# Kernel optimization log

Measured on AMD Instinct MI355X. Metric: run time of the kernel, lower is better.

Reference implementation:

```python
import jax, jax.numpy as jnp
import numpy as np

B, T, C, K, NC = 256, 240, 512, 64, 4  # batch, chunk_size, dim, clusters, num_classes+1
EPS = 1e-12


def setup_inputs() -> dict:
    key = jax.random.key(0)
    k1, k2, k3, k4 = jax.random.split(key, 4)
    inputs = jax.random.normal(k1, (B, T, C), dtype=jnp.float32)
    conv_w = jax.random.normal(k2, (K, C), dtype=jnp.float32) * 0.05   # 1x1 assignment conv, no bias (vladv2=False)
    centroids = jax.random.normal(k3, (K, C), dtype=jnp.float32)
    fc_w = jax.random.normal(k4, (NC, K * C), dtype=jnp.float32) * 0.02
    fc_b = jnp.zeros((NC,), dtype=jnp.float32)
    return {"inputs": inputs, "conv_w": conv_w, "centroids": centroids, "fc_w": fc_w, "fc_b": fc_b}


def _l2norm(x, axis):
    return x / jnp.clip(jnp.linalg.norm(x, axis=axis, keepdims=True), EPS)


def reference(inputs, conv_w, centroids, fc_w, fc_b):
    # inputs: [B, T, C]. Torch permutes to NCHW=(B, C, T, 1); feature dim = C.
    x = _l2norm(inputs, axis=-1)                      # normalize_input over feature dim
    # soft assignment: 1x1 conv -> logits [B, T, K], softmax over clusters
    a = jax.nn.softmax(jnp.einsum('btc,kc->btk', x, conv_w), axis=-1)
    # vlad[b,k,c] = sum_t a[b,t,k] * (x[b,t,c] - centroids[k,c])
    #            = einsum(a, x) - (sum_t a) * centroids   (avoids [B,K,C,T] intermediate)
    vlad = jnp.einsum('btk,btc->bkc', a, x) - a.sum(axis=1)[:, :, None] * centroids[None]
    vlad = _l2norm(vlad, axis=-1)                     # intra-normalization over C
    v = vlad.reshape(vlad.shape[0], -1)               # [B, K*C]
    v = _l2norm(v, axis=-1)                           # final L2 normalize
    # dropout is identity in eval mode; fc + sigmoid
    return jax.nn.sigmoid(v @ fc_w.T + fc_b)
```

## Files before the change

### kernel.cpp

```cpp
#include <hip/hip_runtime.h>
#include <hip/hip_bf16.h>
#include <stdint.h>

#define BB 256
#define TT 240
#define CC 512
#define KK 64
#define NCLS 4
#define CHUNK 32
#define NCHUNK 8
#define THREADS 1024

typedef __attribute__((ext_vector_type(8))) short bf16x8;
typedef __attribute__((ext_vector_type(4))) float f32x4;

__device__ __forceinline__ unsigned short f2bf(float f) {
    union { float f; unsigned int i; } x; x.f = f;
    unsigned int r = x.i + 0x7FFFu + ((x.i >> 16) & 1u);
    return (unsigned short)(r >> 16);
}
__device__ __forceinline__ unsigned int pk2cvt(float lo, float hi) {
    union { __hip_bfloat162 h; unsigned int u; } c;
    c.h = __float22bfloat162_rn(float2{lo, hi});
    return c.u;
}
__device__ __forceinline__ void LB() {
    asm volatile("s_waitcnt lgkmcnt(0)\n\ts_barrier" ::: "memory");
}

struct alignas(16) SMemChunk {
    unsigned short x[CHUNK][520];
    unsigned short xT[CC][40];
    float logitsP[2][CHUNK][68];
    unsigned short aT[KK][40];
};
struct alignas(16) SMemEpi { unsigned short vbuf[KK * CC]; };
union SMemU { SMemChunk c; SMemEpi e; };

__global__ __launch_bounds__(THREADS, 4) void netvlad_kernel(
    const float* __restrict__ inp,
    const float* __restrict__ convw,
    const float* __restrict__ cent,
    const float* __restrict__ fcw,
    const float* __restrict__ fcb,
    float* __restrict__ out)
{
    __shared__ SMemU sm;
    __shared__ float sumsq_sh[CHUNK];
    __shared__ float asum[KK];
    __shared__ float ssred[4][KK];
    __shared__ float gred[16];
    __shared__ float fcred[16][NCLS];
    __shared__ float vinv_sh;

    const int tid  = threadIdx.x;
    const int b    = blockIdx.x;
    const int w    = tid >> 6;
    const int lane = tid & 63;
    const int grp  = (lane >> 4) & 3;
    const int col  = lane & 15;
    const int cg   = w & 3;
    const int th   = (w >> 2) & 1;
    const int kh   = w >> 3;
    const int cq   = w >> 2;

    if (tid < KK) asum[tid] = 0.f;

    f32x4 acc[8];
    #pragma unroll
    for (int j = 0; j < 8; ++j) acc[j] = (f32x4){0.f, 0.f, 0.f, 0.f};

    bf16x8 cw[8];
    #pragma unroll
    for (int s = 0; s < 8; ++s) {
        const float* p = convw + (size_t)(cg * 16 + col) * CC + (kh * 8 + s) * 32 + grp * 8;
        float4 a0 = *(const float4*)p;
        float4 a1 = *(const float4*)(p + 4);
        bf16x8 v;
        v[0] = (short)f2bf(a0.x); v[1] = (short)f2bf(a0.y);
        v[2] = (short)f2bf(a0.z); v[3] = (short)f2bf(a0.w);
        v[4] = (short)f2bf(a1.x); v[5] = (short)f2bf(a1.y);
        v[6] = (short)f2bf(a1.z); v[7] = (short)f2bf(a1.w);
        cw[s] = v;
    }

    const size_t ibase = (size_t)b * (TT * CC);

    float4 r0[2], r1[2];
    #pragma unroll
    for (int i = 0; i < 2; ++i) {
        int g = tid + i * THREADS;
        int t = g >> 6, c8 = (g & 63) << 3;
        const float* p = inp + ibase + (size_t)t * CC + c8;
        r0[i] = *(const float4*)p;
        r1[i] = *(const float4*)(p + 4);
    }

    for (int ch = 0; ch < NCHUNK; ++ch) {
        const int t0 = ch * CHUNK;
        const int tvalid = (TT - t0 < CHUNK) ? (TT - t0) : CHUNK;

        #pragma unroll
        for (int i = 0; i < 2; ++i) {
            int g = tid + i * THREADS;
            int t = g >> 6, c8 = (g & 63) << 3;
            float4 u0 = r0[i], u1 = r1[i];
            uint4 val = (uint4){pk2cvt(u0.x, u0.y), pk2cvt(u0.z, u0.w),
                                pk2cvt(u1.x, u1.y), pk2cvt(u1.z, u1.w)};
            float s = u0.x*u0.x + u0.y*u0.y + u0.z*u0.z + u0.w*u0.w
                    + u1.x*u1.x + u1.y*u1.y + u1.z*u1.z + u1.w*u1.w;
            if (t >= tvalid) { val = (uint4){0u,0u,0u,0u}; s = 0.f; }
            *(uint4*)&sm.c.x[t][c8] = val;
            s += __shfl_xor(s, 1);  s += __shfl_xor(s, 2);  s += __shfl_xor(s, 4);
            s += __shfl_xor(s, 8);  s += __shfl_xor(s, 16); s += __shfl_xor(s, 32);
            if (lane == 0) sumsq_sh[t] = s;
        }
        if (ch + 1 < NCHUNK) {
            int nt0 = t0 + CHUNK;
            #pragma unroll
            for (int i = 0; i < 2; ++i) {
                int g = tid + i * THREADS;
                int t = g >> 6, c8 = (g & 63) << 3;
                int gt = nt0 + t; if (gt > TT - 1) gt = TT - 1;
                const float* p = inp + ibase + (size_t)gt * CC + c8;
                r0[i] = *(const float4*)p;
                r1[i] = *(const float4*)(p + 4);
            }
        }
        LB();

        {
            int c = tid & 511, th2 = tid >> 9;
            #pragma unroll
            for (int tb2 = 0; tb2 < 2; ++tb2) {
                int tb = th2 * 2 + tb2;
                bf16x8 v;
                #pragma unroll
                for (int j = 0; j < 8; ++j) v[j] = (short)sm.c.x[tb * 8 + j][c];
                *(bf16x8*)&sm.c.xT[c][tb * 8] = v;
            }
        }
        {
            f32x4 lt = (f32x4){0.f, 0.f, 0.f, 0.f};
            #pragma unroll
            for (int s = 0; s < 8; ++s) {
                bf16x8 bb = *(const bf16x8*)&sm.c.x[th * 16 + col][(kh * 8 + s) * 32 + grp * 8];
                lt = __builtin_amdgcn_mfma_f32_16x16x32_bf16(cw[s], bb, lt, 0, 0, 0);
            }
            #pragma unroll
            for (int r = 0; r < 4; ++r)
                sm.c.logitsP[kh][th * 16 + col][cg * 16 + grp * 4 + r] = lt[r];
        }
        LB();

        if (tid < 512) {
            int t = tid >> 4, part = tid & 15;
            float rinv = 1.f / fmaxf(sqrtf(sumsq_sh[t]), 1e-12f);
            rinv = (t < tvalid) ? rinv : 0.f;

            float l[4]; float lmax = -1e30f;
            #pragma unroll
            for (int q = 0; q < 4; ++q) {
                l[q] = (sm.c.logitsP[0][t][q * 16 + part] +
                        sm.c.logitsP[1][t][q * 16 + part]) * rinv;
                lmax = fmaxf(lmax, l[q]);
            }
            lmax = fmaxf(lmax, __shfl_xor(lmax, 1));
            lmax = fmaxf(lmax, __shfl_xor(lmax, 2));
            lmax = fmaxf(lmax, __shfl_xor(lmax, 4));
            lmax = fmaxf(lmax, __shfl_xor(lmax, 8));
            float es = 0.f;
            #pragma unroll
            for (int q = 0; q < 4; ++q) { l[q] = __expf(l[q] - lmax); es += l[q]; }
            es += __shfl_xor(es, 1); es += __shfl_xor(es, 2);
            es += __shfl_xor(es, 4); es += __shfl_xor(es, 8);
            float is = 1.f / es;
            #pragma unroll
            for (int q = 0; q < 4; ++q) {
                float a = l[q] * is;
                sm.c.logitsP[0][t][q * 16 + part] = a;
                sm.c.aT[q * 16 + part][t] = (unsigned short)f2bf(a * rinv);
            }
        }
        LB();

        if (tid < KK) {
            float s = 0.f;
            for (int t = 0; t < tvalid; ++t) s += sm.c.logitsP[0][t][tid];
            asum[tid] += s;
        }
        {
            bf16x8 af = *(const bf16x8*)&sm.c.aT[cg * 16 + col][grp * 8];
            #pragma unroll
            for (int j = 0; j < 8; ++j) {
                bf16x8 bf = *(const bf16x8*)&sm.c.xT[cq * 128 + j * 16 + col][grp * 8];
                acc[j] = __builtin_amdgcn_mfma_f32_16x16x32_bf16(af, bf, acc[j], 0, 0, 0);
            }
        }
    }

    LB();

    #pragma unroll
    for (int r = 0; r < 4; ++r) {
        int cl = cg * 16 + grp * 4 + r;
        float as = asum[cl];
        float ss = 0.f;
        #pragma unroll
        for (int j = 0; j < 8; ++j) {
            int c = cq * 128 + j * 16 + col;
            float v = acc[j][r] - as * cent[(size_t)cl * CC + c];
            acc[j][r] = v;
            ss += v * v;
        }
        ss += __shfl_xor(ss, 1); ss += __shfl_xor(ss, 2);
        ss += __shfl_xor(ss, 4); ss += __shfl_xor(ss, 8);
        if (col == 0) ssred[cq][cl] = ss;
    }
    LB();

    float contrib = 0.f;
    #pragma unroll
    for (int r = 0; r < 4; ++r) {
        int cl = cg * 16 + grp * 4 + r;
        float ss = ssred[0][cl] + ssred[1][cl] + ssred[2][cl] + ssred[3][cl];
        float inv = 1.f / fmaxf(sqrtf(ss), 1e-12f);
        #pragma unroll
        for (int j = 0; j < 8; ++j) {
            float v = acc[j][r] * inv;
            acc[j][r] = v;
            contrib += v * v;
        }
    }
    #pragma unroll
    for (int m = 1; m < 64; m <<= 1) contrib += __shfl_xor(contrib, m);
    if (lane == 0) gred[w] = contrib;
    LB();
    if (tid == 0) {
        float tot = 0.f;
        #pragma unroll
        for (int i = 0; i < 16; ++i) tot += gred[i];
        vinv_sh = 1.f / fmaxf(sqrtf(tot), 1e-12f);
    }
    LB();

    {
        float vinv = vinv_sh;
        #pragma unroll
        for (int r = 0; r < 4; ++r) {
            int cl = cg * 16 + grp * 4 + r;
            #pragma unroll
            for (int j = 0; j < 8; ++j) {
                int c = cq * 128 + j * 16 + col;
                sm.e.vbuf[cl * CC + c] = f2bf(acc[j][r] * vinv);
            }
        }
    }
    LB();

    float pacc[NCLS] = {0.f, 0.f, 0.f, 0.f};
    #pragma unroll
    for (int i = 0; i < 4; ++i) {
        int idx = i * 8192 + tid * 8;
        bf16x8 vv = *(const bf16x8*)&sm.e.vbuf[idx];
        float vf[8];
        #pragma unroll
        for (int h = 0; h < 8; ++h) {
            union { unsigned int u; float f; } cvt;
            cvt.u = ((unsigned int)(unsigned short)vv[h]) << 16;
            vf[h] = cvt.f;
        }
        #pragma unroll
        for (int nc = 0; nc < NCLS; ++nc) {
            const float* wp = fcw + (size_t)nc * (KK * CC) + idx;
            float4 w0 = *(const float4*)wp;
            float4 w1 = *(const float4*)(wp + 4);
            pacc[nc] += vf[0] * w0.x + vf[1] * w0.y + vf[2] * w0.z + vf[3] * w0.w
                      + vf[4] * w1.x + vf[5] * w1.y + vf[6] * w1.z + vf[7] * w1.w;
        }
    }
    #pragma unroll
    for (int nc = 0; nc < NCLS; ++nc) {
        #pragma unroll
        for (int m = 1; m < 64; m <<= 1) pacc[nc] += __shfl_xor(pacc[nc], m);
    }
    if (lane == 0) {
        #pragma unroll
        for (int nc = 0; nc < NCLS; ++nc) fcred[w][nc] = pacc[nc];
    }
    LB();
    if (tid < NCLS) {
        float s = fcb[tid];
        #pragma unroll
        for (int ww = 0; ww < 16; ++ww) s += fcred[ww][tid];
        out[b * NCLS + tid] = 1.f / (1.f + __expf(-s));
    }
}

extern "C" void kernel_launch(void* const* d_in, const int* in_sizes, int n_in,
                              void* d_out, int out_size, void* d_ws, size_t ws_size,
                              hipStream_t stream) {
    const float* inp   = (const float*)d_in[0];
    const float* convw = (const float*)d_in[1];
    const float* cent  = (const float*)d_in[2];
    const float* fcw   = (const float*)d_in[3];
    const float* fcb   = (const float*)d_in[4];
    float* o = (float*)d_out;
    netvlad_kernel<<<BB, THREADS, 0, stream>>>(inp, convw, cent, fcw, fcb, o);
}
```

Baseline: 206.3 us.

## Use blocked LDS layout with transpose reads and double-buffered x tile

Replaces the explicit LDS transpose of the x chunk (x -> xT) with a blocked bf16 layout read through ds_read_b64_tr_b16 transpose loads for the aT·x MFMA. Double-buffers the x tile so the next chunk's store does not overwrite data still being read. Moves the per-row sum-of-squares reduction out of the load phase into the softmax threads, merged with the max shuffle reduction. This drops one LDS pass and a set of shuffles per chunk, at the cost of more complex addressing and inline asm that depends on the transpose-read instruction's semantics.

```diff
diff --git a/kernel.cpp b/kernel.cpp
--- a/kernel.cpp
+++ b/kernel.cpp
@@ -11,8 +11,13 @@
 #define NCHUNK 8
 #define THREADS 1024
 
+#define CBS 72
+#define TBS 2312
+#define XELEMS (8 * TBS)
+
 typedef __attribute__((ext_vector_type(8))) short bf16x8;
 typedef __attribute__((ext_vector_type(4))) float f32x4;
+typedef __attribute__((ext_vector_type(2))) unsigned int u32x2;
 
 __device__ __forceinline__ unsigned short f2bf(float f) {
     union { float f; unsigned int i; } x; x.f = f;
@@ -29,10 +34,10 @@
 }
 
 struct alignas(16) SMemChunk {
-    unsigned short x[CHUNK][520];
-    unsigned short xT[CC][40];
-    float logitsP[2][CHUNK][68];
+    unsigned short x[2][XELEMS];
+    float logitsP[2][CHUNK][67];
     unsigned short aT[KK][40];
+    float sumsqP[CHUNK][68];
 };
 struct alignas(16) SMemEpi { unsigned short vbuf[KK * CC]; };
 union SMemU { SMemChunk c; SMemEpi e; };
@@ -46,7 +51,6 @@
     float* __restrict__ out)
 {
     __shared__ SMemU sm;
-    __shared__ float sumsq_sh[CHUNK];
     __shared__ float asum[KK];
     __shared__ float ssred[4][KK];
     __shared__ float gred[16];
@@ -99,6 +103,8 @@
     for (int ch = 0; ch < NCHUNK; ++ch) {
         const int t0 = ch * CHUNK;
         const int tvalid = (TT - t0 < CHUNK) ? (TT - t0) : CHUNK;
+        const int buf = ch & 1;
+        unsigned short* xb = sm.c.x[buf];
 
         #pragma unroll
         for (int i = 0; i < 2; ++i) {
@@ -110,10 +116,9 @@
             float s = u0.x*u0.x + u0.y*u0.y + u0.z*u0.z + u0.w*u0.w
                     + u1.x*u1.x + u1.y*u1.y + u1.z*u1.z + u1.w*u1.w;
             if (t >= tvalid) { val = (uint4){0u,0u,0u,0u}; s = 0.f; }
-            *(uint4*)&sm.c.x[t][c8] = val;
-            s += __shfl_xor(s, 1);  s += __shfl_xor(s, 2);  s += __shfl_xor(s, 4);
-            s += __shfl_xor(s, 8);  s += __shfl_xor(s, 16); s += __shfl_xor(s, 32);
-            if (lane == 0) sumsq_sh[t] = s;
+            int off = (t >> 2) * TBS + (c8 >> 4) * CBS + (t & 3) * 16 + (c8 & 15);
+            *(uint4*)&xb[off] = val;
+            sm.c.sumsqP[t][lane] = s;
         }
         if (ch + 1 < NCHUNK) {
             int nt0 = t0 + CHUNK;
@@ -130,50 +135,45 @@
         LB();
 
         {
-            int c = tid & 511, th2 = tid >> 9;
-            #pragma unroll
-            for (int tb2 = 0; tb2 < 2; ++tb2) {
-                int tb = th2 * 2 + tb2;
-                bf16x8 v;
-                #pragma unroll
-                for (int j = 0; j < 8; ++j) v[j] = (short)sm.c.x[tb * 8 + j][c];
-                *(bf16x8*)&sm.c.xT[c][tb * 8] = v;
-            }
-        }
-        {
             f32x4 lt = (f32x4){0.f, 0.f, 0.f, 0.f};
+            const int t = th * 16 + col;
+            const int rb = (t >> 2) * TBS + (t & 3) * 16 + ((grp & 1) << 3);
             #pragma unroll
             for (int s = 0; s < 8; ++s) {
-                bf16x8 bb = *(const bf16x8*)&sm.c.x[th * 16 + col][(kh * 8 + s) * 32 + grp * 8];
+                const bf16x8 bb = *(const bf16x8*)&xb[rb + ((kh * 8 + s) * 2 + (grp >> 1)) * CBS];
                 lt = __builtin_amdgcn_mfma_f32_16x16x32_bf16(cw[s], bb, lt, 0, 0, 0);
             }
             #pragma unroll
             for (int r = 0; r < 4; ++r)
-                sm.c.logitsP[kh][th * 16 + col][cg * 16 + grp * 4 + r] = lt[r];
+                sm.c.logitsP[kh][t][cg * 16 + grp * 4 + r] = lt[r];
         }
         LB();
 
         if (tid < 512) {
             int t = tid >> 4, part = tid & 15;
-            float rinv = 1.f / fmaxf(sqrtf(sumsq_sh[t]), 1e-12f);
+            float4 sp = *(const float4*)&sm.c.sumsqP[t][part * 4];
+            float ss = sp.x + sp.y + sp.z + sp.w;
+
+            float l[4]; float lmax = -1e30f;
+            #pragma unroll
+            for (int q = 0; q < 4; ++q) {
+                l[q] = sm.c.logitsP[0][t][q * 16 + part] +
+                       sm.c.logitsP[1][t][q * 16 + part];
+                lmax = fmaxf(lmax, l[q]);
+            }
+            #pragma unroll
+            for (int m = 1; m < 16; m <<= 1) {
+                lmax = fmaxf(lmax, __shfl_xor(lmax, m));
+                ss  += __shfl_xor(ss, m);
+            }
+            float rinv = 1.f / fmaxf(sqrtf(ss), 1e-12f);
             rinv = (t < tvalid) ? rinv : 0.f;
-
-            float l[4]; float lmax = -1e30f;
-            #pragma unroll
-            for (int q = 0; q < 4; ++q) {
-                l[q] = (sm.c.logitsP[0][t][q * 16 + part] +
-                        sm.c.logitsP[1][t][q * 16 + part]) * rinv;
-                lmax = fmaxf(lmax, l[q]);
-            }
-            lmax = fmaxf(lmax, __shfl_xor(lmax, 1));
-            lmax = fmaxf(lmax, __shfl_xor(lmax, 2));
-            lmax = fmaxf(lmax, __shfl_xor(lmax, 4));
-            lmax = fmaxf(lmax, __shfl_xor(lmax, 8));
+            float m0 = lmax * rinv;
             float es = 0.f;
             #pragma unroll
-            for (int q = 0; q < 4; ++q) { l[q] = __expf(l[q] - lmax); es += l[q]; }
-            es += __shfl_xor(es, 1); es += __shfl_xor(es, 2);
-            es += __shfl_xor(es, 4); es += __shfl_xor(es, 8);
+            for (int q = 0; q < 4; ++q) { l[q] = __expf(l[q] * rinv - m0); es += l[q]; }
+            #pragma unroll
+            for (int m = 1; m < 16; m <<= 1) es += __shfl_xor(es, m);
             float is = 1.f / es;
             #pragma unroll
             for (int q = 0; q < 4; ++q) {
@@ -191,10 +191,27 @@
         }
         {
             bf16x8 af = *(const bf16x8*)&sm.c.aT[cg * 16 + col][grp * 8];
-            #pragma unroll
-            for (int j = 0; j < 8; ++j) {
-                bf16x8 bf = *(const bf16x8*)&sm.c.xT[cq * 128 + j * 16 + col][grp * 8];
-                acc[j] = __builtin_amdgcn_mfma_f32_16x16x32_bf16(af, bf, acc[j], 0, 0, 0);
+            unsigned xvb = (unsigned)(uintptr_t)&xb[(grp * 2) * TBS + (cq * 8) * CBS + col];
+            #pragma unroll
+            for (int hh = 0; hh < 2; ++hh) {
+                u32x2 lo[4], hi[4];
+                #pragma unroll
+                for (int j2 = 0; j2 < 4; ++j2) {
+                    const unsigned o = (unsigned)((hh * 4 + j2) * 2 * CBS);
+                    asm volatile("ds_read_b64_tr_b16 %0, %1"
+                                 : "=v"(lo[j2]) : "v"(xvb + o));
+                    asm volatile("ds_read_b64_tr_b16 %0, %1"
+                                 : "=v"(hi[j2]) : "v"(xvb + o + (unsigned)(2 * TBS)));
+                }
+                asm volatile("s_waitcnt lgkmcnt(0)" ::: "memory");
+                __builtin_amdgcn_sched_barrier(0);
+                #pragma unroll
+                for (int j2 = 0; j2 < 4; ++j2) {
+                    union { bf16x8 v; u32x2 u[2]; } pk;
+                    pk.u[0] = lo[j2]; pk.u[1] = hi[j2];
+                    acc[hh * 4 + j2] = __builtin_amdgcn_mfma_f32_16x16x32_bf16(
+                        af, pk.v, acc[hh * 4 + j2], 0, 0, 0);
+                }
             }
         }
     }
```

Result: no change. 204.6 us (-0.9%).
